# Performance work log

Hardware: AMD Instinct MI355X
Metric: run time of the kernel (lower is better)

## Reference

```python
import jax, jax.numpy as jnp
import numpy as np

NEG = -1e9


def _ln(x, g, b):
    m = x.mean(-1, keepdims=True)
    v = ((x - m) ** 2).mean(-1, keepdims=True)
    return (x - m) / jnp.sqrt(v + 1e-5) * g + b


def _block(single, pair, single_mask, pair_mask,
           pa_ln_g, pa_ln_b, pa_wqkv, pa_wg, pa_wout,
           pt_ln_g, pt_ln_b, pt_w1, pt_b1, pt_w2, pt_b2,
           sa_ln_g, sa_ln_b, sa_wq, sa_wkv, sa_wb, sa_wout,
           st_ln_g, st_ln_b, st_w1, st_b1, st_w2, st_b2):
    B, L, _, D = pair.shape
    H = sa_wb.shape[1]
    hd = D // H
    scale = 1.0 / jnp.sqrt(jnp.asarray(hd, dtype=pair.dtype))
    # ---- PairUpdate: PairAttention over L*L pseudo-tokens ----
    z = _ln(pair, pa_ln_g, pa_ln_b)                       # [B,L,L,D]
    N = L * L
    qkv = (z @ pa_wqkv).reshape(B, N, 3, H, hd)
    q = qkv[:, :, 0].transpose(0, 2, 1, 3)                # [B,H,N,hd]
    k = qkv[:, :, 1].transpose(0, 2, 1, 3)
    v = qkv[:, :, 2].transpose(0, 2, 1, 3)
    attn = jnp.einsum('bhid,bhjd->bhij', q, k) * scale    # [B,H,N,N]
    pm = pair_mask.reshape(B, 1, N)
    m = pm[:, :, :, None] * pm[:, :, None, :]             # [B,1,N,N]
    attn = jnp.where(m > 0, attn, NEG)
    attn = jax.nn.softmax(attn, axis=-1)
    out = jnp.einsum('bhij,bhjd->bhid', attn, v)          # [B,H,N,hd]
    out = out.transpose(0, 2, 1, 3).reshape(B, L, L, D)
    g = jax.nn.sigmoid(z @ pa_wg)
    out = (out @ pa_wout) * g * pair_mask[..., None]
    pair = pair + out
    t = _ln(pair, pt_ln_g, pt_ln_b)
    t = jax.nn.relu(t @ pt_w1 + pt_b1) @ pt_w2 + pt_b2
    pair = pair + t * pair_mask[..., None]
    # ---- SingleUpdate: AttentionPairBias ----
    s = _ln(single, sa_ln_g, sa_ln_b)                     # [B,L,D]
    q = (s @ sa_wq).reshape(B, L, H, hd)
    kv = (s @ sa_wkv).reshape(B, L, 2, H, hd)
    k2, v2 = kv[:, :, 0], kv[:, :, 1]
    attn = jnp.einsum('bihd,bjhd->bhij', q, k2) * scale   # [B,H,L,L]
    bias = (pair @ sa_wb).transpose(0, 3, 1, 2)           # [B,H,L,L]
    attn = attn + bias
    sm = single_mask[:, None, None, :]
    attn = jnp.where(sm > 0, attn, NEG)
    attn = jax.nn.softmax(attn, axis=-1)
    out = jnp.einsum('bhij,bjhd->bihd', attn, v2).reshape(B, L, D)
    single = single + (out @ sa_wout) * single_mask[..., None]
    # single transition
    t = _ln(single, st_ln_g, st_ln_b)
    t = jax.nn.relu(t @ st_w1 + st_b1) @ st_w2 + st_b2
    single = single + t * single_mask[..., None]
    return single, pair


def setup_inputs() -> dict:
    key = jax.random.key(0)
    B, L, D, H = 1, 64, 144, 8
    ks = iter(jax.random.split(key, 40))
    def nrm(shape, scale=0.02):
        return jax.random.normal(next(ks), shape, dtype=jnp.float32) * scale
    sm = jnp.ones((B, L), jnp.float32).at[:, L - 8:].set(0.0)
    pm = sm[:, :, None] * sm[:, None, :]
    return dict(
        single=jax.random.normal(next(ks), (B, L, D), jnp.float32),
        pair=jax.random.normal(next(ks), (B, L, L, D), jnp.float32),
        single_mask=sm,
        pair_mask=pm,
        pa_ln_g=jnp.ones((D,), jnp.float32), pa_ln_b=jnp.zeros((D,), jnp.float32),
        pa_wqkv=nrm((D, 3 * D)), pa_wg=nrm((D, D)), pa_wout=nrm((D, D)),
        pt_ln_g=jnp.ones((D,), jnp.float32), pt_ln_b=jnp.zeros((D,), jnp.float32),
        pt_w1=nrm((D, 4 * D)), pt_b1=jnp.zeros((4 * D,), jnp.float32),
        pt_w2=nrm((4 * D, D)), pt_b2=jnp.zeros((D,), jnp.float32),
        sa_ln_g=jnp.ones((D,), jnp.float32), sa_ln_b=jnp.zeros((D,), jnp.float32),
        sa_wq=nrm((D, D)), sa_wkv=nrm((D, 2 * D)), sa_wb=nrm((D, H)), sa_wout=nrm((D, D)),
        st_ln_g=jnp.ones((D,), jnp.float32), st_ln_b=jnp.zeros((D,), jnp.float32),
        st_w1=nrm((D, 4 * D)), st_b1=jnp.zeros((4 * D,), jnp.float32),
        st_w2=nrm((4 * D, D)), st_b2=jnp.zeros((D,), jnp.float32),
    )


def reference(single, pair, single_mask, pair_mask,
              pa_ln_g, pa_ln_b, pa_wqkv, pa_wg, pa_wout,
              pt_ln_g, pt_ln_b, pt_w1, pt_b1, pt_w2, pt_b2,
              sa_ln_g, sa_ln_b, sa_wq, sa_wkv, sa_wb, sa_wout,
              st_ln_g, st_ln_b, st_w1, st_b1, st_w2, st_b2):
    return _block(single, pair, single_mask, pair_mask,
                  pa_ln_g, pa_ln_b, pa_wqkv, pa_wg, pa_wout,
                  pt_ln_g, pt_ln_b, pt_w1, pt_b1, pt_w2, pt_b2,
                  sa_ln_g, sa_ln_b, sa_wq, sa_wkv, sa_wb, sa_wout,
                  st_ln_g, st_ln_b, st_w1, st_b1, st_w2, st_b2)
```

## Files before the change

### kernel.cpp

```cpp
#include <hip/hip_runtime.h>
#include <hip/hip_bf16.h>

typedef __hip_bfloat16 bf16;
typedef __attribute__((ext_vector_type(8))) short short8;
typedef __attribute__((ext_vector_type(16))) float floatx16;
typedef __attribute__((ext_vector_type(4))) unsigned int uint4v;

__device__ __forceinline__ float tof(bf16 x){ return __bfloat162float(x); }
__device__ __forceinline__ float bflo(unsigned u){ return __uint_as_float(u<<16); }
__device__ __forceinline__ float bfhi(unsigned u){ return __uint_as_float(u & 0xFFFF0000u); }
__device__ __forceinline__ float ldT(const void* p, long i, bool isf){
  return isf ? ((const float*)p)[i] : tof(((const bf16*)p)[i]);
}
__device__ __forceinline__ void stT(void* p, long i, bool isf, float v){
  if (isf) ((float*)p)[i] = v; else ((bf16*)p)[i] = __float2bfloat16(v);
}

#define LL 64
#define DD 144
#define NN 4096
#define HH 8
#define HDIM 18
#define SCALE 0.23570226039551584f
#define LOG2E 1.4426950408889634f

__global__ __launch_bounds__(256) void prep_weights(const unsigned* __restrict__ smaskw,
    int* __restrict__ dflag,
    const void* __restrict__ wqkv, const void* __restrict__ wg,
    const void* __restrict__ wout, const void* __restrict__ w1, const void* __restrict__ w2,
    const void* __restrict__ swq, const void* __restrict__ swkv,
    const void* __restrict__ swout, const void* __restrict__ sw1, const void* __restrict__ sw2,
    bf16* __restrict__ F1, bf16* __restrict__ Fout, bf16* __restrict__ Fw1,
    bf16* __restrict__ Fw2, bf16* __restrict__ Fs1, bf16* __restrict__ Wtswout,
    bf16* __restrict__ Wtst1, bf16* __restrict__ Wtst2){
  bool isf = (smaskw[0] == 0x3F800000u);
  if (blockIdx.x==0 && threadIdx.x==0) dflag[0] = isf ? 4 : 2;
  long t = (long)blockIdx.x*256 + threadIdx.x;
  if (t < 82944){
    int j=t&7, lane=(int)((t>>3)&63); long tk=t>>9; int ks=tk%9, tile=tk/9;
    int col=tile*32+(lane&31); int k=ks*16+(lane>>5)*8+j;
    float v = (col<432)? ldT(wqkv,(long)k*432+col,isf) : ldT(wg,(long)k*144+(col-432),isf);
    F1[t]=__float2bfloat16(v); return;
  } t -= 82944;
  if (t < 23040){
    int j=t&7, lane=(int)((t>>3)&63); long tk=t>>9; int ks=tk%9, tile=tk/9;
    int col=tile*32+(lane&31); if (col>143) col=143;
    int k=ks*16+(lane>>5)*8+j;
    Fout[t]=__float2bfloat16(ldT(wout,(long)k*144+col,isf)); return;
  } t -= 23040;
  if (t < 82944){
    int j=t&7, lane=(int)((t>>3)&63); long tk=t>>9; int ks=tk%9, tile=tk/9;
    int col=tile*32+(lane&31); int k=ks*16+(lane>>5)*8+j;
    Fw1[t]=__float2bfloat16(ldT(w1,(long)k*576+col,isf)); return;
  } t -= 82944;
  if (t < 92160){
    int j=t&7, lane=(int)((t>>3)&63); long tk=t>>9; int ks=tk%36, tile=tk/36;
    int col=tile*32+(lane&31); if (col>143) col=143;
    int k=ks*16+(lane>>5)*8+j;
    Fw2[t]=__float2bfloat16(ldT(w2,(long)k*144+col,isf)); return;
  } t -= 92160;
  if (t < 64512){
    int j=t&7, lane=(int)((t>>3)&63); long tk=t>>9; int ks=tk%9, tile=tk/9;
    int col=tile*32+(lane&31); if (col>431) col=431;
    int k=ks*16+(lane>>5)*8+j;
    float v = (col<144)? ldT(swq,(long)k*144+col,isf) : ldT(swkv,(long)k*288+(col-144),isf);
    Fs1[t]=__float2bfloat16(v); return;
  } t -= 64512;
  if (t < 20736){ int c=t/144,k=t-(long)c*144; Wtswout[t]=__float2bfloat16(ldT(swout,(long)k*144+c,isf)); return; }
  t -= 20736;
  if (t < 82944){ int c=t/144,k=t-(long)c*144; Wtst1[t]=__float2bfloat16(ldT(sw1,(long)k*576+c,isf)); return; }
  t -= 82944;
  if (t < 82944){ int c=t/576,k=t-(long)c*576; Wtst2[t]=__float2bfloat16(ldT(sw2,(long)k*144+c,isf)); return; }
}

__global__ __launch_bounds__(256) void gemm_fused1(const int* __restrict__ df,
    const void* __restrict__ pairv, const void* __restrict__ lng, const void* __restrict__ lnb,
    const bf16* __restrict__ F1,
    const void* __restrict__ pmask,
    bf16* __restrict__ Qb, bf16* __restrict__ Kf, bf16* __restrict__ Vf,
    bf16* __restrict__ gbuf,
    const void* __restrict__ singlev, const void* __restrict__ sag, const void* __restrict__ sab,
    const bf16* __restrict__ Fs1,
    bf16* __restrict__ q_sb, bf16* __restrict__ kv_sb){
  __shared__ short As[64*152];
  bool isf = df[0]==4;
  int tid=threadIdx.x, lane=tid&63, l31=lane&31, w=tid>>6, wr=w>>1, wc=w&1;
  int g=(lane>>5)*8;

  if (blockIdx.y == 64){
    if (blockIdx.x >= 7) return;
    for (int rr=w; rr<64; rr+=4){
      long base=(long)rr*DD;
      float e0=ldT(singlev,base+lane,isf), e1=ldT(singlev,base+lane+64,isf);
      float e2=(lane<16)?ldT(singlev,base+lane+128,isf):0.f;
      float s=e0+e1+e2;
      #pragma unroll
      for (int o=32;o;o>>=1) s += __shfl_xor(s,o);
      float mean=s*(1.f/144.f);
      float d0=e0-mean, d1=e1-mean, d2=(lane<16)?(e2-mean):0.f;
      float v=d0*d0+d1*d1+d2*d2;
      #pragma unroll
      for (int o=32;o;o>>=1) v += __shfl_xor(v,o);
      float rstd=rsqrtf(v*(1.f/144.f)+1e-5f);
      bf16 h0=__float2bfloat16(d0*rstd*ldT(sag,lane,isf)+ldT(sab,lane,isf));
      bf16 h1=__float2bfloat16(d1*rstd*ldT(sag,lane+64,isf)+ldT(sab,lane+64,isf));
      As[rr*152+lane]=*reinterpret_cast<short*>(&h0);
      As[rr*152+lane+64]=*reinterpret_cast<short*>(&h1);
      if (lane<16){
        bf16 h2=__float2bfloat16(d2*rstd*ldT(sag,lane+128,isf)+ldT(sab,lane+128,isf));
        As[rr*152+lane+128]=*reinterpret_cast<short*>(&h2);
      }
    }
    __syncthreads();
    int tile = blockIdx.x*2 + wc;
    const short8* wf = (const short8*)Fs1;
    floatx16 acc;
    #pragma unroll
    for (int i=0;i<16;i++) acc[i]=0.f;
    #pragma unroll
    for (int ks=0; ks<9; ks++){
      short8 af = *(const short8*)&As[(l31+32*wr)*152 + ks*16 + g];
      acc = __builtin_amdgcn_mfma_f32_32x32x16_bf16(af, wf[(tile*9+ks)*64+lane], acc, 0,0,0);
    }
    int col = tile*32 + l31;
    if (col < 432){
      #pragma unroll
      for (int r=0;r<16;r++){
        int row = 32*wr + (r&3)+8*(r>>2)+4*(lane>>5);
        if (col<144) q_sb[(size_t)row*DD+col] = __float2bfloat16(acc[r]);
        else kv_sb[(size_t)row*288+(col-144)] = __float2bfloat16(acc[r]);
      }
    }
    return;
  }

  int row0 = blockIdx.y*64, col0 = blockIdx.x*64;
  for (int rr=w; rr<64; rr+=4){
    long base=(long)(row0+rr)*DD;
    float e0=ldT(pairv,base+lane,isf), e1=ldT(pairv,base+lane+64,isf);
    float e2=(lane<16)?ldT(pairv,base+lane+128,isf):0.f;
    float s=e0+e1+e2;
    #pragma unroll
    for (int o=32;o;o>>=1) s += __shfl_xor(s,o);
    float mean=s*(1.f/144.f);
    float d0=e0-mean, d1=e1-mean, d2=(lane<16)?(e2-mean):0.f;
    float v=d0*d0+d1*d1+d2*d2;
    #pragma unroll
    for (int o=32;o;o>>=1) v += __shfl_xor(v,o);
    float rstd=rsqrtf(v*(1.f/144.f)+1e-5f);
    bf16 h0=__float2bfloat16(d0*rstd*ldT(lng,lane,isf)+ldT(lnb,lane,isf));
    bf16 h1=__float2bfloat16(d1*rstd*ldT(lng,lane+64,isf)+ldT(lnb,lane+64,isf));
    As[rr*152+lane]=*reinterpret_cast<short*>(&h0);
    As[rr*152+lane+64]=*reinterpret_cast<short*>(&h1);
    if (lane<16){
      bf16 h2=__float2bfloat16(d2*rstd*ldT(lng,lane+128,isf)+ldT(lnb,lane+128,isf));
      As[rr*152+lane+128]=*reinterpret_cast<short*>(&h2);
    }
  }
  __syncthreads();
  int tile = blockIdx.x*2 + wc;
  const short8* wf = (const short8*)F1;
  floatx16 acc;
  #pragma unroll
  for (int i=0;i<16;i++) acc[i]=0.f;
  #pragma unroll
  for (int ks=0; ks<9; ks++){
    short8 af = *(const short8*)&As[(l31+32*wr)*152 + ks*16 + g];
    acc = __builtin_amdgcn_mfma_f32_32x32x16_bf16(af, wf[(tile*9+ks)*64+lane], acc, 0,0,0);
  }
  int col = col0 + wc*32 + l31;
  #pragma unroll
  for (int r=0;r<16;r++){
    int row = row0 + 32*wr + (r&3)+8*(r>>2)+4*(lane>>5);
    if (col < 144){
      int hh = col/18, d = col - hh*18;
      Qb[((size_t)hh*NN+row)*32 + d] = __float2bfloat16(acc[r]*(SCALE*LOG2E));
    } else if (col < 288){
      int c2 = col-144, hh = c2/18, d = c2 - hh*18;
      int f = d>>4, rem = d&15, gs = rem>>3, j = rem&7;
      Kf[((((size_t)hh*128 + (row>>5))*2 + f)*64 + gs*32 + (row&31))*8 + j]
        = __float2bfloat16(acc[r]);
    } else if (col < 432){
      int c2 = col-288, hh = c2/18, d = c2 - hh*18;
      float pm = (ldT(pmask,row,isf)>0.f)?1.f:0.f;
      int kin = row&31, f = kin>>4, k15 = kin&15;
      int gs = (k15>>2)&1, j = (k15&3) | (((k15>>3)&1)<<2);
      Vf[((((size_t)hh*128 + (row>>5))*2 + f)*64 + gs*32 + d)*8 + j]
        = __float2bfloat16(acc[r]*pm);
    } else {
      int c2 = col-432;
      float gt = 1.f/(1.f+__expf(fminf(-acc[r],30.f)));
      gbuf[(size_t)row*DD+c2] = __float2bfloat16(gt);
    }
  }
  if (blockIdx.x==0){
    for (int t=threadIdx.x; t<64*8*7; t+=256){
      int n = row0 + t/56; int rem = t%56; int hh = rem/7, dw = rem%7 + 9;
      ((unsigned*)(Qb + ((size_t)hh*NN+n)*32))[dw] = 0;
    }
    for (int t=threadIdx.x; t<64*8; t+=256){
      int n = row0 + (t>>3), hh = t&7;
      float pm = (ldT(pmask,n,isf)>0.f)?1.f:0.f;
      int kin = n&31, f = kin>>4, k15 = kin&15;
      int gs = (k15>>2)&1, j = (k15&3) | (((k15>>3)&1)<<2);
      Vf[((((size_t)hh*128 + (n>>5))*2 + f)*64 + gs*32 + 18)*8 + j] = __float2bfloat16(pm);
    }
  }
}

__global__ __launch_bounds__(256) void pair_attn_mfma(const int* __restrict__ df,
    const bf16* __restrict__ Qb, const bf16* __restrict__ Kf,
    const bf16* __restrict__ Vf, bf16* __restrict__ aob){
  __shared__ float Comb[4][32][20];
  int h = blockIdx.x & 7, qp2 = blockIdx.x >> 3;
  int qtA = qp2*2, qtB = qp2*2+1;
  int tid = threadIdx.x;
  int w = tid >> 6, lane = tid & 63;
  int l31 = lane & 31, gsel = lane>>5;

  const unsigned* qpA = (const unsigned*)(Qb + ((size_t)h*NN + qtA*32 + l31)*32);
  const unsigned* qpB = (const unsigned*)(Qb + ((size_t)h*NN + qtB*32 + l31)*32);
  short8 qa0, qa1, qb0, qb1;
  #pragma unroll
  for (int j=0;j<4;j++){
    ((unsigned*)&qa0)[j] = qpA[gsel*4+j];
    ((unsigned*)&qa1)[j] = qpA[8+gsel*4+j];
    ((unsigned*)&qb0)[j] = qpB[gsel*4+j];
    ((unsigned*)&qb1)[j] = qpB[8+gsel*4+j];
  }

  floatx16 oA, oB;
  #pragma unroll
  for (int i=0;i<16;i++){ oA[i]=0.f; oB[i]=0.f; }

  const short8* kf8 = (const short8*)Kf + (size_t)h*16384;
  const short8* vf8 = (const short8*)Vf + (size_t)h*16384;
  int c0 = w*32;

  short8 af0 = kf8[(c0*2+0)*64 + lane];
  short8 af1 = kf8[(c0*2+1)*64 + lane];
  short8 av0 = vf8[(c0*2+0)*64 + lane];
  short8 av1 = vf8[(c0*2+1)*64 + lane];

  for (int cc=0; cc<32; cc++){
    int cn = c0 + (cc<31 ? cc+1 : 31);
    short8 naf0 = kf8[(cn*2+0)*64 + lane];
    short8 naf1 = kf8[(cn*2+1)*64 + lane];
    short8 nav0 = vf8[(cn*2+0)*64 + lane];
    short8 nav1 = vf8[(cn*2+1)*64 + lane];

    floatx16 s;
    short8 P1, P2;
    #pragma unroll
    for (int i=0;i<16;i++) s[i]=0.f;
    __builtin_amdgcn_s_setprio(1);
    s = __builtin_amdgcn_mfma_f32_32x32x16_bf16(af0, qa0, s, 0,0,0);
    s = __builtin_amdgcn_mfma_f32_32x32x16_bf16(af1, qa1, s, 0,0,0);
    __builtin_amdgcn_s_setprio(0);
    #pragma unroll
    for (int j=0;j<4;j++){
      unsigned e0 = __float_as_uint(__builtin_amdgcn_exp2f(s[2*j]));
      unsigned e1 = __float_as_uint(__builtin_amdgcn_exp2f(s[2*j+1]));
      ((unsigned*)&P1)[j] = (e0>>16) | (e1 & 0xFFFF0000u);
      unsigned e2 = __float_as_uint(__builtin_amdgcn_exp2f(s[8+2*j]));
      unsigned e3 = __float_as_uint(__builtin_amdgcn_exp2f(s[9+2*j]));
      ((unsigned*)&P2)[j] = (e2>>16) | (e3 & 0xFFFF0000u);
    }
    __builtin_amdgcn_s_setprio(1);
    oA = __builtin_amdgcn_mfma_f32_32x32x16_bf16(av0, P1, oA, 0,0,0);
    oA = __builtin_amdgcn_mfma_f32_32x32x16_bf16(av1, P2, oA, 0,0,0);
    __builtin_amdgcn_s_setprio(0);
    #pragma unroll
    for (int i=0;i<16;i++) s[i]=0.f;
    __builtin_amdgcn_s_setprio(1);
    s = __builtin_amdgcn_mfma_f32_32x32x16_bf16(af0, qb0, s, 0,0,0);
    s = __builtin_amdgcn_mfma_f32_32x32x16_bf16(af1, qb1, s, 0,0,0);
    __builtin_amdgcn_s_setprio(0);
    #pragma unroll
    for (int j=0;j<4;j++){
      unsigned e0 = __float_as_uint(__builtin_amdgcn_exp2f(s[2*j]));
      unsigned e1 = __float_as_uint(__builtin_amdgcn_exp2f(s[2*j+1]));
      ((unsigned*)&P1)[j] = (e0>>16) | (e1 & 0xFFFF0000u);
      unsigned e2 = __float_as_uint(__builtin_amdgcn_exp2f(s[8+2*j]));
      unsigned e3 = __float_as_uint(__builtin_amdgcn_exp2f(s[9+2*j]));
      ((unsigned*)&P2)[j] = (e2>>16) | (e3 & 0xFFFF0000u);
    }
    __builtin_amdgcn_s_setprio(1);
    oB = __builtin_amdgcn_mfma_f32_32x32x16_bf16(av0, P1, oB, 0,0,0);
    oB = __builtin_amdgcn_mfma_f32_32x32x16_bf16(av1, P2, oB, 0,0,0);
    __builtin_amdgcn_s_setprio(0);

    af0=naf0; af1=naf1; av0=nav0; av1=nav1;
  }

  #pragma unroll
  for (int r=0;r<16;r++){
    int d = (r&3) + 8*(r>>2) + 4*gsel;
    if (d < 20) Comb[w][l31][d] = oA[r];
  }
  __syncthreads();
  for (int t=tid; t<32*HDIM; t+=256){
    int q = t/HDIM, d = t-q*HDIM;
    float num = Comb[0][q][d]+Comb[1][q][d]+Comb[2][q][d]+Comb[3][q][d];
    float den = Comb[0][q][18]+Comb[1][q][18]+Comb[2][q][18]+Comb[3][q][18];
    aob[(size_t)(qtA*32+q)*DD + h*HDIM + d] = __float2bfloat16(num/fmaxf(den,1e-20f));
  }
  __syncthreads();
  #pragma unroll
  for (int r=0;r<16;r++){
    int d = (r&3) + 8*(r>>2) + 4*gsel;
    if (d < 20) Comb[w][l31][d] = oB[r];
  }
  __syncthreads();
  for (int t=tid; t<32*HDIM; t+=256){
    int q = t/HDIM, d = t-q*HDIM;
    float num = Comb[0][q][d]+Comb[1][q][d]+Comb[2][q][d]+Comb[3][q][d];
    float den = Comb[0][q][18]+Comb[1][q][18]+Comb[2][q][18]+Comb[3][q][18];
    aob[(size_t)(qtB*32+q)*DD + h*HDIM + d] = __float2bfloat16(num/fmaxf(den,1e-20f));
  }
}

__global__ __launch_bounds__(512) void pair_tail(const int* __restrict__ df,
    const bf16* __restrict__ aob, const bf16* __restrict__ gbuf,
    const void* __restrict__ pairv, const void* __restrict__ pmaskv,
    const bf16* __restrict__ Fout, const void* __restrict__ ptln_g, const void* __restrict__ ptln_b,
    const bf16* __restrict__ Fw1, const void* __restrict__ b1v,
    const bf16* __restrict__ Fw2, const void* __restrict__ b2v,
    const void* __restrict__ wb, void* __restrict__ outP, long outOff,
    float* __restrict__ biasb){
  __shared__ __align__(16) char smem[65536];
  float* p1  = (float*)smem;
  short* ts  = (short*)(smem + 18432);
  short* hh_ = (short*)(smem + 28160);
  float* outv = (float*)(smem + 28160);

  bool isf = df[0]==4;
  int tid=threadIdx.x, lane=tid&63, l31=lane&31, gsel=lane>>5, g=gsel*8;
  int w=tid>>6;
  int r0 = blockIdx.x*32;
  const short8* foutf = (const short8*)Fout;
  const short8* fw1f  = (const short8*)Fw1;
  const short8* fw2f  = (const short8*)Fw2;

  for (int t=tid; t<32*72; t+=512){
    int m=t/72, dw=t%72;
    ((unsigned*)ts)[m*76+dw] = ((const unsigned*)(aob + (size_t)(r0+m)*144))[dw];
  }
  __syncthreads();

  for (int tile=w; tile<5; tile+=8){
    int c0=tile*32;
    floatx16 acc;
    #pragma unroll
    for (int i=0;i<16;i++) acc[i]=0.f;
    #pragma unroll
    for (int ks=0; ks<9; ks++){
      short8 af = *(const short8*)&ts[l31*152 + ks*16 + g];
      acc = __builtin_amdgcn_mfma_f32_32x32x16_bf16(af, foutf[(tile*9+ks)*64+lane], acc, 0,0,0);
    }
    if (c0+l31 < 144){
      #pragma unroll
      for (int r=0;r<16;r++){
        int row=(r&3)+8*(r>>2)+4*gsel;
        p1[row*144 + c0+l31] = acc[r];
      }
    }
  }
  __syncthreads();
  for (int t=tid; t<32*144; t+=512){
    int row=t/144; int col=t-row*144;
    long gidx=(long)(r0+row)*144 + col;
    float pm = (ldT(pmaskv, r0+row, isf)>0.f)?1.f:0.f;
    p1[t] = ldT(pairv,gidx,isf) + p1[t]*tof(gbuf[gidx])*pm;
  }
  __syncthreads();
  for (int rr=w; rr<32; rr+=8){
    float e0=p1[rr*144+lane], e1=p1[rr*144+lane+64], e2=(lane<16)?p1[rr*144+lane+128]:0.f;
    float s=e0+e1+e2;
    #pragma unroll
    for (int o=32;o;o>>=1) s += __shfl_xor(s,o);
    float mean=s*(1.f/144.f);
    float d0=e0-mean, d1=e1-mean, d2=(lane<16)?(e2-mean):0.f;
    float v=d0*d0+d1*d1+d2*d2;
    #pragma unroll
    for (int o=32;o;o>>=1) v += __shfl_xor(v,o);
    float rstd=rsqrtf(v*(1.f/144.f)+1e-5f);
    bf16 h0 = __float2bfloat16(d0*rstd*ldT(ptln_g,lane,isf)    + ldT(ptln_b,lane,isf));
    bf16 h1 = __float2bfloat16(d1*rstd*ldT(ptln_g,lane+64,isf) + ldT(ptln_b,lane+64,isf));
    ts[rr*152+lane]    = *reinterpret_cast<short*>(&h0);
    ts[rr*152+lane+64] = *reinterpret_cast<short*>(&h1);
    if (lane<16){
      bf16 h2 = __float2bfloat16(d2*rstd*ldT(ptln_g,lane+128,isf) + ldT(ptln_b,lane+128,isf));
      ts[rr*152+lane+128] = *reinterpret_cast<short*>(&h2);
    }
  }
  __syncthreads();
  for (int tile=w; tile<18; tile+=8){
    int c0=tile*32, colB=c0+l31;
    floatx16 acc;
    #pragma unroll
    for (int i=0;i<16;i++) acc[i]=0.f;
    #pragma unroll
    for (int ks=0; ks<9; ks++){
      short8 af = *(const short8*)&ts[l31*152 + ks*16 + g];
      acc = __builtin_amdgcn_mfma_f32_32x32x16_bf16(af, fw1f[(tile*9+ks)*64+lane], acc, 0,0,0);
    }
    float bb = ldT(b1v,colB,isf);
    #pragma unroll
    for (int r=0;r<16;r++){
      int row=(r&3)+8*(r>>2)+4*gsel;
      bf16 hv = __float2bfloat16(fmaxf(acc[r]+bb,0.f));
      hh_[row*584 + colB] = *reinterpret_cast<short*>(&hv);
    }
  }
  __syncthreads();
  floatx16 fin; int fc0 = -1;
  for (int tile=w; tile<5; tile+=8){
    int c0=tile*32;
    int colB=c0+l31; if (colB>143) colB=143;
    floatx16 acc;
    #pragma unroll
    for (int i=0;i<16;i++) acc[i]=0.f;
    #pragma unroll
    for (int ks=0; ks<36; ks++){
      short8 af = *(const short8*)&hh_[l31*584 + ks*16 + g];
      acc = __builtin_amdgcn_mfma_f32_32x32x16_bf16(af, fw2f[(tile*36+ks)*64+lane], acc, 0,0,0);
    }
    float bb = ldT(b2v,colB,isf);
    #pragma unroll
    for (int r=0;r<16;r++){
      int row=(r&3)+8*(r>>2)+4*gsel;
      float pm = (ldT(pmaskv, r0+row, isf)>0.f)?1.f:0.f;
      float val = p1[row*144 + colB] + (acc[r]+bb)*pm;
      if (c0+l31 < 144)
        stT(outP, outOff + (long)(r0+row)*144 + c0+l31, isf, val);
      fin[r]=val;
    }
    fc0 = c0;
  }
  __syncthreads();
  if (fc0 >= 0 && fc0+l31 < 144){
    #pragma unroll
    for (int r=0;r<16;r++){
      int row=(r&3)+8*(r>>2)+4*gsel;
      outv[row*144 + fc0+l31] = fin[r];
    }
  }
  __syncthreads();
  if (tid < 256){
    int n = tid>>3, hb = tid&7;
    float acc=0.f;
    #pragma unroll 4
    for (int k=0;k<144;k++) acc += outv[n*144+k]*ldT(wb,k*8+hb,isf);
    biasb[(size_t)(r0+n)*8+hb]=acc;
  }
}

__global__ __launch_bounds__(512) void single_tail(const int* __restrict__ df,
    const void* __restrict__ single, const bf16* __restrict__ q_sb,
    const bf16* __restrict__ kv_sb, const float* __restrict__ biasb,
    const void* __restrict__ smask, const bf16* __restrict__ Wtswout,
    const void* __restrict__ stln_g, const void* __restrict__ stln_b,
    const bf16* __restrict__ Wtst1, const void* __restrict__ st_b1,
    const bf16* __restrict__ Wtst2, const void* __restrict__ st_b2,
    void* __restrict__ outS){
  bool isf = df[0]==4;
  __shared__ __align__(16) short kvs[64*288];
  __shared__ float pexp[512];
  __shared__ float tot[8];
  __shared__ __align__(16) float bb[512];
  __shared__ float part[576];
  __shared__ float qs[DD], as_[DD], s1v[DD], tss[DD], hs[576];
  __shared__ float mr[2];
  int n = blockIdx.x, tid = threadIdx.x;
  {
    const uint4v* src = (const uint4v*)kv_sb;
    uint4v* dst = (uint4v*)kvs;
    for (int t=tid; t<2304; t+=512) dst[t] = src[t];
  }
  if (tid<DD) qs[tid] = tof(q_sb[(size_t)n*DD+tid]);
  {
    const uint4v* src = (const uint4v*)(biasb + (size_t)n*512);
    uint4v* dst = (uint4v*)bb;
    if (tid<128) dst[tid] = src[tid];
  }
  __syncthreads();
  {
    int h = tid>>6, j = tid&63;
    const unsigned* kr = (const unsigned*)&kvs[j*288 + h*HDIM];
    float s=0.f;
    #pragma unroll
    for (int i=0;i<9;i++){
      unsigned u = kr[i];
      s += qs[h*HDIM+2*i]*bflo(u) + qs[h*HDIM+2*i+1]*bfhi(u);
    }
    s = fminf(s*SCALE + bb[j*8+h], 30.f);
    pexp[tid] = (ldT(smask,j,isf)>0.f) ? __expf(s) : 0.f;
  }
  __syncthreads();
  if (tid<64){
    int h=tid>>3, j0=(tid&7)*8;
    float t2=0.f;
    #pragma unroll
    for (int j=0;j<8;j++) t2 += pexp[h*64+j0+j];
    #pragma unroll
    for (int o=4;o;o>>=1) t2 += __shfl_xor(t2,o);
    if ((tid&7)==0) tot[h] = fmaxf(t2,1e-20f);
  }
  __syncthreads();
  for (int t=tid; t<576; t+=512){
    int seg=t/144, d=t-seg*144, h=d/HDIM, j0=seg*16;
    float a0=0.f, a1=0.f;
    #pragma unroll
    for (int j=0;j<16;j+=2){
      unsigned u0 = ((unsigned)(unsigned short)kvs[(j0+j)*288 + 144 + d])<<16;
      unsigned u1 = ((unsigned)(unsigned short)kvs[(j0+j+1)*288 + 144 + d])<<16;
      a0 += pexp[h*64+j0+j]*__uint_as_float(u0);
      a1 += pexp[h*64+j0+j+1]*__uint_as_float(u1);
    }
    part[seg*144+d]=a0+a1;
  }
  __syncthreads();
  if (tid<DD){
    int h = tid/HDIM;
    as_[tid] = (part[tid]+part[144+tid]+part[288+tid]+part[432+tid])/tot[h];
  }
  __syncthreads();
  float sm = ldT(smask,n,isf);
  if (tid<288){
    int seg=tid/144, d=tid-seg*144;
    const uint4v* wr = (const uint4v*)(Wtswout + (size_t)d*DD) + seg*9;
    int b0=seg*72;
    float a=0.f;
    #pragma unroll
    for (int kw=0; kw<9; kw++){
      uint4v u = wr[kw]; int e=b0+8*kw;
      a += as_[e]*bflo(u[0]) + as_[e+1]*bfhi(u[0])
         + as_[e+2]*bflo(u[1]) + as_[e+3]*bfhi(u[1])
         + as_[e+4]*bflo(u[2]) + as_[e+5]*bfhi(u[2])
         + as_[e+6]*bflo(u[3]) + as_[e+7]*bfhi(u[3]);
    }
    part[seg*144+d]=a;
  }
  __syncthreads();
  if (tid<DD) s1v[tid] = ldT(single,(long)n*DD+tid,isf) + (part[tid]+part[144+tid])*sm;
  __syncthreads();
  if (tid < 64){
    float e0 = s1v[tid], e1 = s1v[tid+64], e2 = (tid<16)?s1v[tid+128]:0.f;
    float s = e0+e1+e2;
    #pragma unroll
    for (int o=32;o;o>>=1) s += __shfl_xor(s,o);
    float mean = s*(1.f/144.f);
    float d0=e0-mean, d1=e1-mean, d2=(tid<16)?(e2-mean):0.f;
    float v = d0*d0+d1*d1+d2*d2;
    #pragma unroll
    for (int o=32;o;o>>=1) v += __shfl_xor(v,o);
    if (tid==0){ mr[0]=mean; mr[1]=rsqrtf(v*(1.f/144.f)+1e-5f); }
  }
  __syncthreads();
  if (tid<DD) tss[tid] = (s1v[tid]-mr[0])*mr[1]*ldT(stln_g,tid,isf) + ldT(stln_b,tid,isf);
  __syncthreads();
  for (int c=tid; c<576; c+=512){
    const uint4v* wr = (const uint4v*)(Wtst1 + (size_t)c*DD);
    float a0=ldT(st_b1,c,isf), a1=0.f;
    #pragma unroll 3
    for (int kw=0; kw<18; kw+=2){
      uint4v u = wr[kw], u2 = wr[kw+1];
      a0 += tss[8*kw+0]*bflo(u[0]) + tss[8*kw+1]*bfhi(u[0])
          + tss[8*kw+2]*bflo(u[1]) + tss[8*kw+3]*bfhi(u[1])
          + tss[8*kw+4]*bflo(u[2]) + tss[8*kw+5]*bfhi(u[2])
          + tss[8*kw+6]*bflo(u[3]) + tss[8*kw+7]*bfhi(u[3]);
      a1 += tss[8*kw+8]*bflo(u2[0]) + tss[8*kw+9]*bfhi(u2[0])
          + tss[8*kw+10]*bflo(u2[1]) + tss[8*kw+11]*bfhi(u2[1])
          + tss[8*kw+12]*bflo(u2[2]) + tss[8*kw+13]*bfhi(u2[2])
          + tss[8*kw+14]*bflo(u2[3]) + tss[8*kw+15]*bfhi(u2[3]);
    }
    hs[c]=fmaxf(a0+a1,0.f);
  }
  __syncthreads();
  for (int t=tid; t<576; t+=512){
    int seg=t/144, d=t-seg*144;
    const uint4v* wr = (const uint4v*)(Wtst2 + (size_t)d*576) + seg*18;
    int b0=seg*144;
    float a0=0.f, a1=0.f;
    #pragma unroll 3
    for (int kw=0; kw<18; kw+=2){
      uint4v u = wr[kw], u2 = wr[kw+1];
      int e=b0+8*kw;
      a0 += hs[e]*bflo(u[0]) + hs[e+1]*bfhi(u[0])
          + hs[e+2]*bflo(u[1]) + hs[e+3]*bfhi(u[1])
          + hs[e+4]*bflo(u[2]) + hs[e+5]*bfhi(u[2])
          + hs[e+6]*bflo(u[3]) + hs[e+7]*bfhi(u[3]);
      a1 += hs[e+8]*bflo(u2[0]) + hs[e+9]*bfhi(u2[0])
          + hs[e+10]*bflo(u2[1]) + hs[e+11]*bfhi(u2[1])
          + hs[e+12]*bflo(u2[2]) + hs[e+13]*bfhi(u2[2])
          + hs[e+14]*bflo(u2[3]) + hs[e+15]*bfhi(u2[3]);
    }
    part[seg*144+d]=a0+a1;
  }
  __syncthreads();
  if (tid<DD)
    stT(outS,(long)n*DD+tid,isf,
        s1v[tid] + (ldT(st_b2,tid,isf)+part[tid]+part[144+tid]+part[288+tid]+part[432+tid])*sm);
}

extern "C" void kernel_launch(void* const* d_in, const int* in_sizes, int n_in,
                              void* d_out, int out_size, void* d_ws, size_t ws_size,
                              hipStream_t stream) {
  char* wsb = (char*)d_ws;
  int*   dflag = (int*)wsb;
  bf16*  F1     = (bf16*)(wsb + 16);
  bf16*  Fout   = F1 + 82944;
  bf16*  Fw1    = Fout + 23040;
  bf16*  Fw2    = Fw1 + 82944;
  bf16*  Fs1    = Fw2 + 92160;
  bf16*  Wtswout= Fs1 + 64512;
  bf16*  Wtst1  = Wtswout + 20736;
  bf16*  Wtst2  = Wtst1 + 82944;
  bf16*  Qb   = Wtst2 + 82944;
  bf16*  Kf   = Qb + (size_t)HH*NN*32;
  bf16*  Vf   = Kf + (size_t)HH*131072;
  bf16*  gbuf = Vf + (size_t)HH*131072;
  bf16*  aob  = gbuf + (size_t)NN*DD;
  float* biasb= (float*)(aob + (size_t)NN*DD);
  bf16*  q_sb = (bf16*)(biasb + NN*8);
  bf16*  kv_sb= q_sb + LL*DD;

  const long OUTP_OFF = (long)LL*DD;

  prep_weights<<<2079,256,0,stream>>>((const unsigned*)d_in[2], dflag,
      d_in[6], d_in[7], d_in[8], d_in[11], d_in[13],
      d_in[17], d_in[18], d_in[20], d_in[23], d_in[25],
      F1, Fout, Fw1, Fw2, Fs1, Wtswout, Wtst1, Wtst2);

  gemm_fused1<<<dim3(9,65),256,0,stream>>>(dflag, d_in[1], d_in[4], d_in[5], F1, d_in[3],
                                           Qb, Kf, Vf, gbuf,
                                           d_in[0], d_in[15], d_in[16], Fs1, q_sb, kv_sb);
  pair_attn_mfma<<<512,256,0,stream>>>(dflag, Qb, Kf, Vf, aob);
  pair_tail<<<128,512,0,stream>>>(dflag, aob, gbuf, d_in[1], d_in[3],
                                  Fout, d_in[9], d_in[10], Fw1, d_in[12],
                                  Fw2, d_in[14], d_in[19], d_out, OUTP_OFF, biasb);
  single_tail<<<LL,512,0,stream>>>(dflag, d_in[0], q_sb, kv_sb, biasb, d_in[2],
                                   Wtswout, d_in[21], d_in[22], Wtst1, d_in[24],
                                   Wtst2, d_in[26], d_out);
  (void)in_sizes; (void)n_in; (void)out_size; (void)ws_size;
}
```

Before: 217.9 us.

## Process four query tiles per attention block and widen pair_tail to 1024 threads

The pair attention kernel now handles four 32-row query tiles per block instead of two, reusing each K/V fragment load for twice as many score/PV MFMAs. The grid is halved to 256 blocks with launch_bounds(256,1). The bf16 packing of exp values switches to a single v_perm. pair_tail is launched with 1024 threads and its strided loops are retuned to 16 waves, though several tile loops have fewer tiles than waves, so more waves sit idle. Risks are one block per CU leaving fewer waves to hide latency in attention, higher register pressure from four accumulators, and possible spills under the 1024-thread bound in pair_tail.

```diff
diff --git a/kernel.cpp b/kernel.cpp
--- a/kernel.cpp
+++ b/kernel.cpp
@@ -208,30 +208,30 @@
   }
 }
 
-__global__ __launch_bounds__(256) void pair_attn_mfma(const int* __restrict__ df,
+__global__ __launch_bounds__(256,1) void pair_attn_mfma(const int* __restrict__ df,
     const bf16* __restrict__ Qb, const bf16* __restrict__ Kf,
     const bf16* __restrict__ Vf, bf16* __restrict__ aob){
   __shared__ float Comb[4][32][20];
-  int h = blockIdx.x & 7, qp2 = blockIdx.x >> 3;
-  int qtA = qp2*2, qtB = qp2*2+1;
+  int h = blockIdx.x & 7, qp4 = blockIdx.x >> 3;
+  int qt0 = qp4*4;
   int tid = threadIdx.x;
   int w = tid >> 6, lane = tid & 63;
   int l31 = lane & 31, gsel = lane>>5;
 
-  const unsigned* qpA = (const unsigned*)(Qb + ((size_t)h*NN + qtA*32 + l31)*32);
-  const unsigned* qpB = (const unsigned*)(Qb + ((size_t)h*NN + qtB*32 + l31)*32);
-  short8 qa0, qa1, qb0, qb1;
+  short8 qf[4][2];
   #pragma unroll
-  for (int j=0;j<4;j++){
-    ((unsigned*)&qa0)[j] = qpA[gsel*4+j];
-    ((unsigned*)&qa1)[j] = qpA[8+gsel*4+j];
-    ((unsigned*)&qb0)[j] = qpB[gsel*4+j];
-    ((unsigned*)&qb1)[j] = qpB[8+gsel*4+j];
-  }
-
-  floatx16 oA, oB;
+  for (int t=0;t<4;t++){
+    const unsigned* qp = (const unsigned*)(Qb + ((size_t)h*NN + (qt0+t)*32 + l31)*32);
+    #pragma unroll
+    for (int j=0;j<4;j++){
+      ((unsigned*)&qf[t][0])[j] = qp[gsel*4+j];
+      ((unsigned*)&qf[t][1])[j] = qp[8+gsel*4+j];
+    }
+  }
+
+  floatx16 o0, o1, o2, o3, zf;
   #pragma unroll
-  for (int i=0;i<16;i++){ oA[i]=0.f; oB[i]=0.f; }
+  for (int i=0;i<16;i++){ o0[i]=0.f; o1[i]=0.f; o2[i]=0.f; o3[i]=0.f; zf[i]=0.f; }
 
   const short8* kf8 = (const short8*)Kf + (size_t)h*16384;
   const short8* vf8 = (const short8*)Vf + (size_t)h*16384;
@@ -249,78 +249,63 @@
     short8 nav0 = vf8[(cn*2+0)*64 + lane];
     short8 nav1 = vf8[(cn*2+1)*64 + lane];
 
-    floatx16 s;
-    short8 P1, P2;
-    #pragma unroll
-    for (int i=0;i<16;i++) s[i]=0.f;
-    __builtin_amdgcn_s_setprio(1);
-    s = __builtin_amdgcn_mfma_f32_32x32x16_bf16(af0, qa0, s, 0,0,0);
-    s = __builtin_amdgcn_mfma_f32_32x32x16_bf16(af1, qa1, s, 0,0,0);
-    __builtin_amdgcn_s_setprio(0);
-    #pragma unroll
-    for (int j=0;j<4;j++){
-      unsigned e0 = __float_as_uint(__builtin_amdgcn_exp2f(s[2*j]));
-      unsigned e1 = __float_as_uint(__builtin_amdgcn_exp2f(s[2*j+1]));
-      ((unsigned*)&P1)[j] = (e0>>16) | (e1 & 0xFFFF0000u);
-      unsigned e2 = __float_as_uint(__builtin_amdgcn_exp2f(s[8+2*j]));
-      unsigned e3 = __float_as_uint(__builtin_amdgcn_exp2f(s[9+2*j]));
-      ((unsigned*)&P2)[j] = (e2>>16) | (e3 & 0xFFFF0000u);
-    }
-    __builtin_amdgcn_s_setprio(1);
-    oA = __builtin_amdgcn_mfma_f32_32x32x16_bf16(av0, P1, oA, 0,0,0);
-    oA = __builtin_amdgcn_mfma_f32_32x32x16_bf16(av1, P2, oA, 0,0,0);
-    __builtin_amdgcn_s_setprio(0);
-    #pragma unroll
-    for (int i=0;i<16;i++) s[i]=0.f;
-    __builtin_amdgcn_s_setprio(1);
-    s = __builtin_amdgcn_mfma_f32_32x32x16_bf16(af0, qb0, s, 0,0,0);
-    s = __builtin_amdgcn_mfma_f32_32x32x16_bf16(af1, qb1, s, 0,0,0);
-    __builtin_amdgcn_s_setprio(0);
-    #pragma unroll
-    for (int j=0;j<4;j++){
-      unsigned e0 = __float_as_uint(__builtin_amdgcn_exp2f(s[2*j]));
-      unsigned e1 = __float_as_uint(__builtin_amdgcn_exp2f(s[2*j+1]));
-      ((unsigned*)&P1)[j] = (e0>>16) | (e1 & 0xFFFF0000u);
-      unsigned e2 = __float_as_uint(__builtin_amdgcn_exp2f(s[8+2*j]));
-      unsigned e3 = __float_as_uint(__builtin_amdgcn_exp2f(s[9+2*j]));
-      ((unsigned*)&P2)[j] = (e2>>16) | (e3 & 0xFFFF0000u);
-    }
-    __builtin_amdgcn_s_setprio(1);
-    oB = __builtin_amdgcn_mfma_f32_32x32x16_bf16(av0, P1, oB, 0,0,0);
-    oB = __builtin_amdgcn_mfma_f32_32x32x16_bf16(av1, P2, oB, 0,0,0);
-    __builtin_amdgcn_s_setprio(0);
+    #pragma unroll
+    for (int t=0;t<4;t++){
+      floatx16 s;
+      short8 P1, P2;
+      __builtin_amdgcn_s_setprio(1);
+      s = __builtin_amdgcn_mfma_f32_32x32x16_bf16(af0, qf[t][0], zf, 0,0,0);
+      s = __builtin_amdgcn_mfma_f32_32x32x16_bf16(af1, qf[t][1], s, 0,0,0);
+      __builtin_amdgcn_s_setprio(0);
+      #pragma unroll
+      for (int j=0;j<4;j++){
+        unsigned e0 = __float_as_uint(__builtin_amdgcn_exp2f(s[2*j]));
+        unsigned e1 = __float_as_uint(__builtin_amdgcn_exp2f(s[2*j+1]));
+        ((unsigned*)&P1)[j] = __builtin_amdgcn_perm(e1, e0, 0x07060302);
+        unsigned e2 = __float_as_uint(__builtin_amdgcn_exp2f(s[8+2*j]));
+        unsigned e3 = __float_as_uint(__builtin_amdgcn_exp2f(s[9+2*j]));
+        ((unsigned*)&P2)[j] = __builtin_amdgcn_perm(e3, e2, 0x07060302);
+      }
+      __builtin_amdgcn_s_setprio(1);
+      if (t==0){
+        o0 = __builtin_amdgcn_mfma_f32_32x32x16_bf16(av0, P1, o0, 0,0,0);
+        o0 = __builtin_amdgcn_mfma_f32_32x32x16_bf16(av1, P2, o0, 0,0,0);
+      } else if (t==1){
+        o1 = __builtin_amdgcn_mfma_f32_32x32x16_bf16(av0, P1, o1, 0,0,0);
+        o1 = __builtin_amdgcn_mfma_f32_32x32x16_bf16(av1, P2, o1, 0,0,0);
+      } else if (t==2){
+        o2 = __builtin_amdgcn_mfma_f32_32x32x16_bf16(av0, P1, o2, 0,0,0);
+        o2 = __builtin_amdgcn_mfma_f32_32x32x16_bf16(av1, P2, o2, 0,0,0);
+      } else {
+        o3 = __builtin_amdgcn_mfma_f32_32x32x16_bf16(av0, P1, o3, 0,0,0);
+        o3 = __builtin_amdgcn_mfma_f32_32x32x16_bf16(av1, P2, o3, 0,0,0);
+      }
+      __builtin_amdgcn_s_setprio(0);
+    }
 
     af0=naf0; af1=naf1; av0=nav0; av1=nav1;
   }
 
   #pragma unroll
-  for (int r=0;r<16;r++){
-    int d = (r&3) + 8*(r>>2) + 4*gsel;
-    if (d < 20) Comb[w][l31][d] = oA[r];
-  }
-  __syncthreads();
-  for (int t=tid; t<32*HDIM; t+=256){
-    int q = t/HDIM, d = t-q*HDIM;
-    float num = Comb[0][q][d]+Comb[1][q][d]+Comb[2][q][d]+Comb[3][q][d];
-    float den = Comb[0][q][18]+Comb[1][q][18]+Comb[2][q][18]+Comb[3][q][18];
-    aob[(size_t)(qtA*32+q)*DD + h*HDIM + d] = __float2bfloat16(num/fmaxf(den,1e-20f));
-  }
-  __syncthreads();
-  #pragma unroll
-  for (int r=0;r<16;r++){
-    int d = (r&3) + 8*(r>>2) + 4*gsel;
-    if (d < 20) Comb[w][l31][d] = oB[r];
-  }
-  __syncthreads();
-  for (int t=tid; t<32*HDIM; t+=256){
-    int q = t/HDIM, d = t-q*HDIM;
-    float num = Comb[0][q][d]+Comb[1][q][d]+Comb[2][q][d]+Comb[3][q][d];
-    float den = Comb[0][q][18]+Comb[1][q][18]+Comb[2][q][18]+Comb[3][q][18];
-    aob[(size_t)(qtB*32+q)*DD + h*HDIM + d] = __float2bfloat16(num/fmaxf(den,1e-20f));
-  }
-}
-
-__global__ __launch_bounds__(512) void pair_tail(const int* __restrict__ df,
+  for (int tt=0;tt<4;tt++){
+    #pragma unroll
+    for (int r=0;r<16;r++){
+      int d = (r&3) + 8*(r>>2) + 4*gsel;
+      float val = (tt==0)?o0[r]:(tt==1)?o1[r]:(tt==2)?o2[r]:o3[r];
+      if (d < 20) Comb[w][l31][d] = val;
+    }
+    __syncthreads();
+    for (int t=tid; t<32*HDIM; t+=256){
+      int q = t/HDIM, d = t-q*HDIM;
+      float num = Comb[0][q][d]+Comb[1][q][d]+Comb[2][q][d]+Comb[3][q][d];
+      float den = Comb[0][q][18]+Comb[1][q][18]+Comb[2][q][18]+Comb[3][q][18];
+      aob[(size_t)((qt0+tt)*32+q)*DD + h*HDIM + d] = __float2bfloat16(num/fmaxf(den,1e-20f));
+    }
+    __syncthreads();
+  }
+}
+
+__global__ __launch_bounds__(1024) void pair_tail(const int* __restrict__ df,
     const bf16* __restrict__ aob, const bf16* __restrict__ gbuf,
     const void* __restrict__ pairv, const void* __restrict__ pmaskv,
     const bf16* __restrict__ Fout, const void* __restrict__ ptln_g, const void* __restrict__ ptln_b,
@@ -342,13 +327,13 @@
   const short8* fw1f  = (const short8*)Fw1;
   const short8* fw2f  = (const short8*)Fw2;
 
-  for (int t=tid; t<32*72; t+=512){
+  for (int t=tid; t<32*72; t+=1024){
     int m=t/72, dw=t%72;
     ((unsigned*)ts)[m*76+dw] = ((const unsigned*)(aob + (size_t)(r0+m)*144))[dw];
   }
   __syncthreads();
 
-  for (int tile=w; tile<5; tile+=8){
+  for (int tile=w; tile<5; tile+=16){
     int c0=tile*32;
     floatx16 acc;
     #pragma unroll
@@ -367,14 +352,14 @@
     }
   }
   __syncthreads();
-  for (int t=tid; t<32*144; t+=512){
+  for (int t=tid; t<32*144; t+=1024){
     int row=t/144; int col=t-row*144;
     long gidx=(long)(r0+row)*144 + col;
     float pm = (ldT(pmaskv, r0+row, isf)>0.f)?1.f:0.f;
     p1[t] = ldT(pairv,gidx,isf) + p1[t]*tof(gbuf[gidx])*pm;
   }
   __syncthreads();
-  for (int rr=w; rr<32; rr+=8){
+  for (int rr=w; rr<32; rr+=16){
     float e0=p1[rr*144+lane], e1=p1[rr*144+lane+64], e2=(lane<16)?p1[rr*144+lane+128]:0.f;
     float s=e0+e1+e2;
     #pragma unroll
@@ -395,7 +380,7 @@
     }
   }
   __syncthreads();
-  for (int tile=w; tile<18; tile+=8){
+  for (int tile=w; tile<18; tile+=16){
     int c0=tile*32, colB=c0+l31;
     floatx16 acc;
     #pragma unroll
@@ -415,7 +400,7 @@
   }
   __syncthreads();
   floatx16 fin; int fc0 = -1;
-  for (int tile=w; tile<5; tile+=8){
+  for (int tile=w; tile<5; tile+=16){
     int c0=tile*32;
     int colB=c0+l31; if (colB>143) colB=143;
     floatx16 acc;
@@ -636,10 +621,10 @@
   gemm_fused1<<<dim3(9,65),256,0,stream>>>(dflag, d_in[1], d_in[4], d_in[5], F1, d_in[3],
                                            Qb, Kf, Vf, gbuf,
                                            d_in[0], d_in[15], d_in[16], Fs1, q_sb, kv_sb);
-  pair_attn_mfma<<<512,256,0,stream>>>(dflag, Qb, Kf, Vf, aob);
-  pair_tail<<<128,512,0,stream>>>(dflag, aob, gbuf, d_in[1], d_in[3],
-                                  Fout, d_in[9], d_in[10], Fw1, d_in[12],
-                                  Fw2, d_in[14], d_in[19], d_out, OUTP_OFF, biasb);
+  pair_attn_mfma<<<256,256,0,stream>>>(dflag, Qb, Kf, Vf, aob);
+  pair_tail<<<128,1024,0,stream>>>(dflag, aob, gbuf, d_in[1], d_in[3],
+                                   Fout, d_in[9], d_in[10], Fw1, d_in[12],
+                                   Fw2, d_in[14], d_in[19], d_out, OUTP_OFF, biasb);
   single_tail<<<LL,512,0,stream>>>(dflag, d_in[0], q_sb, kv_sb, biasb, d_in[2],
                                    Wtswout, d_in[21], d_in[22], Wtst1, d_in[24],
                                    Wtst2, d_in[26], d_out);
```

Measured after the change: 225.2 us. 3.4% more time.
